# Kernel tuning notes

Hardware: AMD Instinct MI355X
Metric: run time of the kernel (lower is better)

Reference implementation:

```python
import jax, jax.numpy as jnp
import numpy as np

B, S, D, H, F = 2, 2048, 768, 12, 3072
HD = D // H


def setup_inputs() -> dict:
    key = jax.random.key(0)
    ks = jax.random.split(key, 6)
    g = lambda k, sh, sc: jax.random.normal(k, sh, jnp.float32) * sc
    return {
        "x": g(ks[0], (B, S, D), 1.0),
        "mask": jnp.tril(jnp.ones((1, 1, S, S), dtype=jnp.bool_)),  # causal
        "qkv_w": g(ks[1], (3 * D, D), 0.02),
        "qkv_b": jnp.zeros((3 * D,), jnp.float32),
        "out_w": g(ks[2], (D, D), 0.02),
        "out_b": jnp.zeros((D,), jnp.float32),
        "fc1_w": g(ks[3], (F, D), 0.02),
        "fc1_b": jnp.zeros((F,), jnp.float32),
        "fc2_w": g(ks[4], (D, F), 0.02),
        "fc2_b": jnp.zeros((D,), jnp.float32),
        "ln1_w": jnp.ones((D,), jnp.float32),
        "ln1_b": jnp.zeros((D,), jnp.float32),
        "ln2_w": jnp.ones((D,), jnp.float32),
        "ln2_b": jnp.zeros((D,), jnp.float32),
    }


def _layernorm(x, w, b, eps=1e-5):
    m = x.mean(-1, keepdims=True)
    v = ((x - m) ** 2).mean(-1, keepdims=True)
    return (x - m) * jax.lax.rsqrt(v + eps) * w + b


def reference(x, mask, qkv_w, qkv_b, out_w, out_b, fc1_w, fc1_b, fc2_w, fc2_b,
              ln1_w, ln1_b, ln2_w, ln2_b):
    b, s, d = x.shape
    h = d // HD  # num_heads
    # --- pre-norm multi-head self-attention (dropout = eval/identity) ---
    hx = _layernorm(x, ln1_w, ln1_b)
    qkv = hx @ qkv_w.T + qkv_b                      # [b,s,3d]
    qkv = qkv.reshape(b, s, 3, h, HD).transpose(2, 0, 3, 1, 4)  # [3,b,h,s,hd]
    q, k, v = qkv[0], qkv[1], qkv[2]
    scale = jnp.sqrt(jnp.float32(HD))
    scores = jnp.einsum("bhqd,bhkd->bhqk", q, k) / scale  # [b,h,s,s]
    scores = jnp.where(mask, scores, -jnp.inf)
    attn = jax.nn.softmax(scores, axis=-1)
    o = jnp.einsum("bhqk,bhkd->bhqd", attn, v)      # [b,h,s,hd]
    o = o.transpose(0, 2, 1, 3).reshape(b, s, d)
    x = x + (o @ out_w.T + out_b)
    # --- pre-norm GELU feed-forward ---
    h2 = _layernorm(x, ln2_w, ln2_b)
    ff = jax.nn.gelu(h2 @ fc1_w.T + fc1_b, approximate=False) @ fc2_w.T + fc2_b
    return x + ff
```

## Files before the change

kernel.cpp:

```cpp
#include <hip/hip_runtime.h>
#include <hip/hip_bf16.h>
#include <cstdint>
#include <cstddef>

typedef __bf16 bf16;
typedef unsigned short ushort_t;
typedef __attribute__((ext_vector_type(8))) __bf16 bf16x8;
typedef __attribute__((ext_vector_type(4))) __bf16 bf16x4;
typedef __attribute__((ext_vector_type(4))) float f32x4;

#define NB 2
#define NS 2048
#define ND 768
#define NH 12
#define NF 3072
#define NT (NB * NS)

__device__ __forceinline__ f32x4 mfma16(bf16x8 a, bf16x8 b, f32x4 c) {
  return __builtin_amdgcn_mfma_f32_16x16x32_bf16(a, b, c, 0, 0, 0);
}

__device__ __forceinline__ void gl_lds16(const bf16* g, bf16* l) {
  __builtin_amdgcn_global_load_lds(
      (__attribute__((address_space(1))) void*)(uintptr_t)g,
      (__attribute__((address_space(3))) void*)l,
      16, 0, 0);
}

__device__ __forceinline__ int xcd_swz(int lin, int nwg) {
  const int q = nwg >> 3, r = nwg & 7;
  const int x = lin & 7, i = lin >> 3;
  return (x < r ? x * (q + 1) : r * (q + 1) + (x - r) * q) + i;
}

__device__ __forceinline__ float gelu_fast(float v) {
  const float u = v * (0.7978845608028654f + 0.03567740814f * v * v);
  const float e = exp2f(u * 2.885390081777927f);
  return v - v / (1.f + e);
}

__global__ __launch_bounds__(256) void sniff_kernel(
    const ushort_t* __restrict__ x, int* __restrict__ flag) {
  __shared__ int s[4];
  int bad = 0;
  for (int i = threadIdx.x; i < 4096; i += 256) {
    const int e = (x[i] >> 7) & 0xFF;
    bad |= (e >= 0xC0);
  }
  bad = __any(bad) ? 1 : 0;
  if ((threadIdx.x & 63) == 0) s[threadIdx.x >> 6] = bad;
  __syncthreads();
  if (threadIdx.x == 0) *flag = s[0] | s[1] | s[2] | s[3];
}

struct CvtArgs {
  const void* s[8];
  bf16* d[8];
  int n8[8];
  int total8;
};

__global__ __launch_bounds__(256) void cvt_all(CvtArgs a,
                                               const int* __restrict__ flag) {
  const int isf = *flag;
  const int stride = gridDim.x * 256;
  for (int i = blockIdx.x * 256 + threadIdx.x; i < a.total8; i += stride) {
    int seg = 0, off = i;
    while (off >= a.n8[seg]) { off -= a.n8[seg]; ++seg; }
    bf16x8 o;
    if (isf) {
      const float* s = (const float*)a.s[seg] + (size_t)off * 8;
      const f32x4 f0 = *(const f32x4*)s;
      const f32x4 f1 = *(const f32x4*)(s + 4);
#pragma unroll
      for (int j = 0; j < 4; ++j) {
        o[j] = (bf16)f0[j];
        o[4 + j] = (bf16)f1[j];
      }
    } else {
      o = *((const bf16x8*)a.s[seg] + off);
    }
    *((bf16x8*)a.d[seg] + off) = o;
  }
}

__global__ __launch_bounds__(256) void ln_kernel(
    const void* __restrict__ xv, const void* __restrict__ wv,
    const void* __restrict__ bv, bf16* __restrict__ y,
    const int* __restrict__ flag) {
  const int isf = *flag;
  const int row = blockIdx.x * 4 + (threadIdx.x >> 6);
  const int L = threadIdx.x & 63;
  const float* xf = (const float*)xv;
  const bf16* xh = (const bf16*)xv;
  const float* wf = (const float*)wv;
  const bf16* wh = (const bf16*)wv;
  const float* bf_ = (const float*)bv;
  const bf16* bh = (const bf16*)bv;
  const size_t base = (size_t)row * ND;
  float v[12];
  float s = 0.f, s2 = 0.f;
#pragma unroll
  for (int i = 0; i < 12; ++i) {
    const int c = L + i * 64;
    v[i] = isf ? xf[base + c] : (float)xh[base + c];
    s += v[i];
    s2 += v[i] * v[i];
  }
#pragma unroll
  for (int off = 1; off < 64; off <<= 1) {
    s += __shfl_xor(s, off);
    s2 += __shfl_xor(s2, off);
  }
  const float mean = s * (1.f / 768.f);
  const float var = s2 * (1.f / 768.f) - mean * mean;
  const float rstd = rsqrtf(var + 1e-5f);
  bf16* yr = y + base;
#pragma unroll
  for (int i = 0; i < 12; ++i) {
    const int c = L + i * 64;
    const float ww = isf ? wf[c] : (float)wh[c];
    const float bb = isf ? bf_[c] : (float)bh[c];
    yr[c] = (bf16)((v[i] - mean) * rstd * ww + bb);
  }
}

__global__ __launch_bounds__(256) void vt_kernel(
    const bf16* __restrict__ qkv, bf16* __restrict__ vT) {
  const int bh = blockIdx.y;
  const int b = bh / NH, h = bh % NH;
  const int st = blockIdx.x;
  __shared__ bf16 Vs[64 * 72];
  const int tid = threadIdx.x;
  {
    const int r = tid >> 2, c = (tid & 3) * 16;
    const bf16* src =
        qkv + (size_t)(b * NS + st * 64 + r) * (3 * ND) + 2 * ND + h * 64 + c;
    *(bf16x8*)&Vs[r * 72 + c] = *(const bf16x8*)src;
    *(bf16x8*)&Vs[r * 72 + c + 8] = *(const bf16x8*)(src + 8);
  }
  __syncthreads();
  {
    const int hd = tid >> 2, t0 = (tid & 3) * 16;
    bf16x8 o0, o1;
#pragma unroll
    for (int j = 0; j < 8; ++j) {
      o0[j] = Vs[(t0 + j) * 72 + hd];
      o1[j] = Vs[(t0 + 8 + j) * 72 + hd];
    }
    bf16* dst = vT + ((size_t)bh * 64 + hd) * NS + st * 64 + t0;
    *(bf16x8*)dst = o0;
    *(bf16x8*)(dst + 8) = o1;
  }
}

template <int EPI>
__global__ __launch_bounds__(256) void gemm64(
    const bf16* __restrict__ A, const bf16* __restrict__ Bt,
    const bf16* __restrict__ bias, const void* resid, void* C,
    int N, int K, int row0, const int* __restrict__ flag) {
  constexpr int NBUF = 3;
  __shared__ bf16 As[NBUF][64 * 64];
  __shared__ bf16 Bs[NBUF][128 * 64];
  int isf = 0;
  if (EPI == 2) {
    isf = *flag;
    asm volatile("" ::"s"(isf));
  }
  const int tid = threadIdx.x;
  const int w = tid >> 6, L = tid & 63;
  const int lg = L >> 4, lc = L & 15;
  const int wm = (w >> 1) * 32, wn = (w & 1) * 64;
  const int nwg = gridDim.x * gridDim.y;
  const int lin = xcd_swz(blockIdx.y * gridDim.x + blockIdx.x, nwg);
  const int bm = lin / gridDim.x, bn = lin % gridDim.x;

  const bf16* Ab = A + (size_t)bm * 64 * K;
  const bf16* Bb = Bt + (size_t)bn * 128 * K;

  const int srw = tid >> 3;
  const int scw = ((tid & 7) ^ (srw & 7)) * 8;

  f32x4 acc[2][4];
#pragma unroll
  for (int i = 0; i < 2; ++i)
#pragma unroll
    for (int j = 0; j < 4; ++j) acc[i][j] = (f32x4){0.f, 0.f, 0.f, 0.f};

#define G64_STAGE(buf, kk)                                                  \
  do {                                                                      \
    gl_lds16(Ab + (size_t)srw * K + (kk) + scw, As[buf] + tid * 8);         \
    gl_lds16(Ab + (size_t)(srw + 32) * K + (kk) + scw,                      \
             As[buf] + 2048 + tid * 8);                                     \
    gl_lds16(Bb + (size_t)srw * K + (kk) + scw, Bs[buf] + tid * 8);         \
    gl_lds16(Bb + (size_t)(srw + 32) * K + (kk) + scw,                      \
             Bs[buf] + 2048 + tid * 8);                                     \
    gl_lds16(Bb + (size_t)(srw + 64) * K + (kk) + scw,                      \
             Bs[buf] + 4096 + tid * 8);                                     \
    gl_lds16(Bb + (size_t)(srw + 96) * K + (kk) + scw,                      \
             Bs[buf] + 6144 + tid * 8);                                     \
  } while (0)

#define G64_COMP(cb)                                                        \
  do {                                                                      \
    bf16x8 af[2][2], bfr[2][4];                                             \
    _Pragma("unroll") for (int kk2 = 0; kk2 < 2; ++kk2) {                   \
      _Pragma("unroll") for (int mt = 0; mt < 2; ++mt) {                    \
        const int ra = wm + mt * 16 + lc;                                   \
        af[kk2][mt] = *(const bf16x8*)&As[cb][ra * 64 +                     \
                                             (((kk2 * 4 + lg) ^ (ra & 7))   \
                                              << 3)];                       \
      }                                                                     \
      _Pragma("unroll") for (int nt = 0; nt < 4; ++nt) {                    \
        const int rb = wn + nt * 16 + lc;                                   \
        bfr[kk2][nt] = *(const bf16x8*)&Bs[cb][rb * 64 +                    \
                                              (((kk2 * 4 + lg) ^ (rb & 7))  \
                                               << 3)];                      \
      }                                                                     \
    }                                                                       \
    _Pragma("unroll") for (int kk2 = 0; kk2 < 2; ++kk2)                     \
        _Pragma("unroll") for (int mt = 0; mt < 2; ++mt)                    \
            _Pragma("unroll") for (int nt = 0; nt < 4; ++nt)                \
                acc[mt][nt] = mfma16(af[kk2][mt], bfr[kk2][nt],             \
                                     acc[mt][nt]);                          \
  } while (0)

  const int nk = K >> 6;
  G64_STAGE(0, 0);
  int cur = 0, stg = 1;
  int k = 0;
  for (; k < nk - 1; ++k) {
    G64_STAGE(stg, (k + 1) * 64);
    asm volatile("s_waitcnt vmcnt(6)" ::: "memory");
    asm volatile("s_barrier" ::: "memory");
    G64_COMP(cur);
    cur = (cur + 1 == NBUF) ? 0 : cur + 1;
    stg = (stg + 1 == NBUF) ? 0 : stg + 1;
  }
  __syncthreads();
  G64_COMP(cur);
#undef G64_STAGE
#undef G64_COMP

  const float* rf = (const float*)resid;
  const bf16* rh = (const bf16*)resid;
  float* Cf = (float*)C;
  bf16* Ch = (bf16*)C;
#pragma unroll
  for (int mt = 0; mt < 2; ++mt) {
#pragma unroll
    for (int nt = 0; nt < 4; ++nt) {
      const int col = bn * 128 + wn + nt * 16 + lc;
      const float bv = (float)bias[col];
#pragma unroll
      for (int r = 0; r < 4; ++r) {
        const int row = bm * 64 + wm + mt * 16 + lg * 4 + r;
        float v = acc[mt][nt][r] + bv;
        if (EPI == 1) v = gelu_fast(v);
        const size_t idx = (size_t)(row0 + row) * N + col;
        if (EPI == 2) {
          v += isf ? rf[idx] : (float)rh[idx];
          if (isf) Cf[idx] = v; else Ch[idx] = (bf16)v;
        } else {
          Ch[idx] = (bf16)v;
        }
      }
    }
  }
}

template <int EPI, int TM>
__global__ __launch_bounds__(256) void gemm_fast(
    const bf16* __restrict__ A, const bf16* __restrict__ Bt,
    const bf16* __restrict__ bias, const void* resid, void* C,
    int N, int K, int row0, const int* __restrict__ flag) {
  constexpr int NBUF = (TM == 64) ? 5 : 3;
  constexpr int LOOK = NBUF - 2;
  constexpr int MT = TM / 32;
  __shared__ bf16 As[NBUF][TM * 32];
  __shared__ bf16 Bs[NBUF][128 * 32];
  int isf = 0;
  if (EPI == 2) {
    isf = *flag;
    asm volatile("" ::"s"(isf));
  }
  const int tid = threadIdx.x;
  const int w = tid >> 6, L = tid & 63;
  const int lg = L >> 4, lc = L & 15;
  const int lgx = (lg ^ ((lc >> 1) & 3)) * 8;
  const int wm = (w >> 1) * (TM / 2), wn = (w & 1) * 64;
  const int nwg = gridDim.x * gridDim.y;
  const int lin = xcd_swz(blockIdx.y * gridDim.x + blockIdx.x, nwg);
  const int bm = lin / gridDim.x, bn = lin % gridDim.x;

  const bf16* Ab = A + (size_t)bm * TM * K;
  const bf16* Bb = Bt + (size_t)bn * 128 * K;

  const int sr = tid >> 2;
  const int sc = ((tid & 3) ^ ((tid >> 3) & 3)) * 8;

  f32x4 acc[MT][4];
#pragma unroll
  for (int i = 0; i < MT; ++i)
#pragma unroll
    for (int j = 0; j < 4; ++j) acc[i][j] = (f32x4){0.f, 0.f, 0.f, 0.f};

#define GF_STAGE(buf, kk)                                                   \
  do {                                                                      \
    gl_lds16(Ab + (size_t)sr * K + (kk) + sc, As[buf] + tid * 8);           \
    if (TM == 128)                                                          \
      gl_lds16(Ab + (size_t)(sr + 64) * K + (kk) + sc,                      \
               As[buf] + 2048 + tid * 8);                                   \
    gl_lds16(Bb + (size_t)sr * K + (kk) + sc, Bs[buf] + tid * 8);           \
    gl_lds16(Bb + (size_t)(sr + 64) * K + (kk) + sc,                        \
             Bs[buf] + 2048 + tid * 8);                                     \
  } while (0)

#define GF_COMP(cb)                                                         \
  do {                                                                      \
    bf16x8 af[MT], bfr[4];                                                  \
    _Pragma("unroll") for (int mt = 0; mt < MT; ++mt) af[mt] =              \
        *(const bf16x8*)&As[cb][(wm + mt * 16 + lc) * 32 + lgx];            \
    _Pragma("unroll") for (int nt = 0; nt < 4; ++nt) bfr[nt] =              \
        *(const bf16x8*)&Bs[cb][(wn + nt * 16 + lc) * 32 + lgx];            \
    _Pragma("unroll") for (int mt = 0; mt < MT; ++mt)                       \
        _Pragma("unroll") for (int nt = 0; nt < 4; ++nt) acc[mt][nt] =      \
            mfma16(af[mt], bfr[nt], acc[mt][nt]);                           \
  } while (0)

  const int nk = K >> 5;
#pragma unroll
  for (int s = 0; s < LOOK; ++s)
    if (s < nk) GF_STAGE(s, s * 32);
  int cur = 0, stg = LOOK;
  int k = 0;
  const int kmain = (nk > LOOK) ? nk - LOOK : 0;
  for (; k < kmain; ++k) {
    GF_STAGE(stg, (k + LOOK) * 32);
    if (TM == 64)
      asm volatile("s_waitcnt vmcnt(9)" ::: "memory");
    else
      asm volatile("s_waitcnt vmcnt(4)" ::: "memory");
    asm volatile("s_barrier" ::: "memory");
    GF_COMP(cur);
    cur = (cur + 1 == NBUF) ? 0 : cur + 1;
    stg = (stg + 1 == NBUF) ? 0 : stg + 1;
  }
  __syncthreads();
  for (; k < nk; ++k) {
    GF_COMP(cur);
    cur = (cur + 1 == NBUF) ? 0 : cur + 1;
  }
#undef GF_STAGE
#undef GF_COMP

  const float* rf = (const float*)resid;
  const bf16* rh = (const bf16*)resid;
  float* Cf = (float*)C;
  bf16* Ch = (bf16*)C;
#pragma unroll
  for (int mt = 0; mt < MT; ++mt) {
#pragma unroll
    for (int nt = 0; nt < 4; ++nt) {
      const int col = bn * 128 + wn + nt * 16 + lc;
      const float bv = (float)bias[col];
#pragma unroll
      for (int r = 0; r < 4; ++r) {
        const int row = bm * TM + wm + mt * 16 + lg * 4 + r;
        float v = acc[mt][nt][r] + bv;
        if (EPI == 1) v = gelu_fast(v);
        const size_t idx = (size_t)(row0 + row) * N + col;
        if (EPI == 2) {
          v += isf ? rf[idx] : (float)rh[idx];
          if (isf) Cf[idx] = v; else Ch[idx] = (bf16)v;
        } else {
          Ch[idx] = (bf16)v;
        }
      }
    }
  }
}

__global__ __launch_bounds__(256) void gemm_qkv(
    const bf16* __restrict__ A, const bf16* __restrict__ Bt,
    const bf16* __restrict__ bias, bf16* __restrict__ qkvout,
    bf16* __restrict__ vT) {
  const int K = ND, N = 3 * ND;
  constexpr int NBUF = 3;
  constexpr int LOOK = 1;
  __shared__ bf16 As[NBUF][128 * 32];
  __shared__ bf16 Bs[NBUF][128 * 32];
  const int tid = threadIdx.x;
  const int w = tid >> 6, L = tid & 63;
  const int lg = L >> 4, lc = L & 15;
  const int lgx = (lg ^ ((lc >> 1) & 3)) * 8;
  const int wm = (w >> 1) * 64, wn = (w & 1) * 64;
  const int nwg = gridDim.x * gridDim.y;
  const int lin = xcd_swz(blockIdx.y * gridDim.x + blockIdx.x, nwg);
  const int bm = lin / gridDim.x, bn = lin % gridDim.x;

  const bf16* Ab = A + (size_t)bm * 128 * K;
  const bf16* Bb = Bt + (size_t)bn * 128 * K;

  const int sr = tid >> 2;
  const int sc = ((tid & 3) ^ ((tid >> 3) & 3)) * 8;

  f32x4 acc[4][4];
#pragma unroll
  for (int i = 0; i < 4; ++i)
#pragma unroll
    for (int j = 0; j < 4; ++j) acc[i][j] = (f32x4){0.f, 0.f, 0.f, 0.f};

#define QKV_STAGE(buf, kk)                                                  \
  do {                                                                      \
    gl_lds16(Ab + (size_t)sr * K + (kk) + sc, As[buf] + tid * 8);           \
    gl_lds16(Ab + (size_t)(sr + 64) * K + (kk) + sc,                        \
             As[buf] + 2048 + tid * 8);                                     \
    gl_lds16(Bb + (size_t)sr * K + (kk) + sc, Bs[buf] + tid * 8);           \
    gl_lds16(Bb + (size_t)(sr + 64) * K + (kk) + sc,                        \
             Bs[buf] + 2048 + tid * 8);                                     \
  } while (0)

#define QKV_COMP(cb)                                                        \
  do {                                                                      \
    bf16x8 af[4], bfr[4];                                                   \
    _Pragma("unroll") for (int mt = 0; mt < 4; ++mt) af[mt] =               \
        *(const bf16x8*)&As[cb][(wm + mt * 16 + lc) * 32 + lgx];            \
    _Pragma("unroll") for (int nt = 0; nt < 4; ++nt) bfr[nt] =              \
        *(const bf16x8*)&Bs[cb][(wn + nt * 16 + lc) * 32 + lgx];            \
    _Pragma("unroll") for (int mt = 0; mt < 4; ++mt)                        \
        _Pragma("unroll") for (int nt = 0; nt < 4; ++nt) acc[mt][nt] =      \
            mfma16(af[mt], bfr[nt], acc[mt][nt]);                           \
  } while (0)

  const int nk = K >> 5;
  QKV_STAGE(0, 0);
  int cur = 0, stg = LOOK;
  int k = 0;
  const int kmain = nk - LOOK;
  for (; k < kmain; ++k) {
    QKV_STAGE(stg, (k + LOOK) * 32);
    asm volatile("s_waitcnt vmcnt(4)" ::: "memory");
    asm volatile("s_barrier" ::: "memory");
    QKV_COMP(cur);
    cur = (cur + 1 == NBUF) ? 0 : cur + 1;
    stg = (stg + 1 == NBUF) ? 0 : stg + 1;
  }
  __syncthreads();
  for (; k < nk; ++k) {
    QKV_COMP(cur);
    cur = (cur + 1 == NBUF) ? 0 : cur + 1;
  }
#undef QKV_STAGE
#undef QKV_COMP

#pragma unroll
  for (int mt = 0; mt < 4; ++mt) {
#pragma unroll
    for (int nt = 0; nt < 4; ++nt) {
      const int col = bn * 128 + wn + nt * 16 + lc;
      const float bv = (float)bias[col];
      if (col < 2 * ND) {
#pragma unroll
        for (int r = 0; r < 4; ++r) {
          const int row = bm * 128 + wm + mt * 16 + lg * 4 + r;
          qkvout[(size_t)row * N + col] = (bf16)(acc[mt][nt][r] + bv);
        }
      } else {
        const int colv = col - 2 * ND;
        const int h_ = colv >> 6, hd = colv & 63;
        bf16x4 pk;
#pragma unroll
        for (int r = 0; r < 4; ++r) pk[r] = (bf16)(acc[mt][nt][r] + bv);
        const int tok0 = bm * 128 + wm + mt * 16 + lg * 4;
        const int b_ = tok0 >> 11, s0 = tok0 & (NS - 1);
        *(bf16x4*)&vT[((size_t)(b_ * NH + h_) * 64 + hd) * NS + s0] = pk;
      }
    }
  }
}

template <int EPI>
__global__ __launch_bounds__(256) void gemm_bt(
    const bf16* __restrict__ A, const void* __restrict__ Bt,
    const void* __restrict__ bias, const void* resid, void* C,
    int N, int K, int row0, const int* __restrict__ flag) {
  __shared__ bf16 As[128 * 32];
  __shared__ bf16 Bs[128 * 32];
  const int isf = *flag;
  const int tid = threadIdx.x;
  const int w = tid >> 6, L = tid & 63;
  const int lg = L >> 4, lc = L & 15;
  const int wm = (w >> 1) * 64, wn = (w & 1) * 64;
  const int nwg = gridDim.x * gridDim.y;
  const int lin = xcd_swz(blockIdx.y * gridDim.x + blockIdx.x, nwg);
  const int bm = lin / gridDim.x, bn = lin % gridDim.x;

  const bf16* Ab = A + (size_t)bm * 128 * K;
  const bf16* Bth = (const bf16*)Bt + (size_t)bn * 128 * K;
  const float* Btf = (const float*)Bt + (size_t)bn * 128 * K;

  const int sr = tid >> 1;
  const int sc = (tid & 1) * 16;

  f32x4 acc[4][4];
#pragma unroll
  for (int i = 0; i < 4; ++i)
#pragma unroll
    for (int j = 0; j < 4; ++j) acc[i][j] = (f32x4){0.f, 0.f, 0.f, 0.f};

  for (int k0 = 0; k0 < K; k0 += 32) {
    const bf16* ap = Ab + (size_t)sr * K + k0 + sc;
    const bf16x8 a0 = *(const bf16x8*)ap;
    const bf16x8 a1 = *(const bf16x8*)(ap + 8);
    bf16x8 b0, b1;
    if (isf) {
      const float* bp = Btf + (size_t)sr * K + k0 + sc;
      const f32x4 f0 = *(const f32x4*)bp;
      const f32x4 f1 = *(const f32x4*)(bp + 4);
      const f32x4 f2 = *(const f32x4*)(bp + 8);
      const f32x4 f3 = *(const f32x4*)(bp + 12);
#pragma unroll
      for (int j = 0; j < 4; ++j) {
        b0[j] = (bf16)f0[j];
        b0[4 + j] = (bf16)f1[j];
        b1[j] = (bf16)f2[j];
        b1[4 + j] = (bf16)f3[j];
      }
    } else {
      const bf16* bp = Bth + (size_t)sr * K + k0 + sc;
      b0 = *(const bf16x8*)bp;
      b1 = *(const bf16x8*)(bp + 8);
    }
    __syncthreads();
    *(bf16x8*)&As[sr * 32 + sc] = a0;
    *(bf16x8*)&As[sr * 32 + sc + 8] = a1;
    *(bf16x8*)&Bs[sr * 32 + sc] = b0;
    *(bf16x8*)&Bs[sr * 32 + sc + 8] = b1;
    __syncthreads();

    bf16x8 af[4], bfr[4];
#pragma unroll
    for (int mt = 0; mt < 4; ++mt)
      af[mt] = *(const bf16x8*)&As[(wm + mt * 16 + lc) * 32 + lg * 8];
#pragma unroll
    for (int nt = 0; nt < 4; ++nt)
      bfr[nt] = *(const bf16x8*)&Bs[(wn + nt * 16 + lc) * 32 + lg * 8];
#pragma unroll
    for (int mt = 0; mt < 4; ++mt)
#pragma unroll
      for (int nt = 0; nt < 4; ++nt)
        acc[mt][nt] = mfma16(af[mt], bfr[nt], acc[mt][nt]);
  }

  const float* biasf = (const float*)bias;
  const bf16* biash = (const bf16*)bias;
  const float* rf = (const float*)resid;
  const bf16* rh = (const bf16*)resid;
  float* Cf = (float*)C;
  bf16* Ch = (bf16*)C;
#pragma unroll
  for (int mt = 0; mt < 4; ++mt) {
#pragma unroll
    for (int nt = 0; nt < 4; ++nt) {
      const int col = bn * 128 + wn + nt * 16 + lc;
      const float bv = isf ? biasf[col] : (float)biash[col];
#pragma unroll
      for (int r = 0; r < 4; ++r) {
        const int row = bm * 128 + wm + mt * 16 + lg * 4 + r;
        float v = acc[mt][nt][r] + bv;
        if (EPI == 1) v = gelu_fast(v);
        const size_t idx = (size_t)(row0 + row) * N + col;
        if (EPI == 2) {
          v += isf ? rf[idx] : (float)rh[idx];
          if (isf) Cf[idx] = v; else Ch[idx] = (bf16)v;
        } else {
          Ch[idx] = (bf16)v;
        }
      }
    }
  }
}

__global__ __launch_bounds__(128) void flash_attn_sp(
    const bf16* __restrict__ qkv, const bf16* __restrict__ vT,
    bf16* __restrict__ o, float* __restrict__ po, float* __restrict__ pl) {
  const int nwg = gridDim.x * gridDim.y;
  const int lin = xcd_swz(blockIdx.y * gridDim.x + blockIdx.x, nwg);
  const int bh = lin / 47;
  const int c = lin % 47;
  const int b = bh / NH, h = bh % NH;
  int qt, kt_lo, kt_hi, direct, cc = 0;
  if (c == 0) {
    qt = 16; kt_lo = 0; kt_hi = 16; direct = 1;
  } else if (c <= 30) {
    qt = 31 - ((c - 1) >> 1);
    const int hh = (qt + 1) >> 1;
    cc = (c - 1) & 1;
    if (cc) { kt_lo = hh; kt_hi = qt; }
    else    { kt_lo = 0;  kt_hi = hh - 1; }
    direct = 0;
  } else {
    qt = 46 - c; kt_lo = 0; kt_hi = qt; direct = 1;
  }
  const int q0 = qt * 64;
  const int tid = threadIdx.x;
  const int w = tid >> 6, L = tid & 63;
  const int lg = L >> 4, lc = L & 15;

  __shared__ bf16 Ks[64 * 72];
  __shared__ bf16 Vts[64 * 72];
  __shared__ bf16 Ps[2][32 * 72];

  const float QSCALE = 0.18033688011112042f;
  bf16x8 qf[2][2];
#pragma unroll
  for (int m = 0; m < 2; ++m) {
    const size_t tokq = (size_t)(b * NS + q0 + w * 32 + m * 16 + lc);
    const bf16* qp = qkv + tokq * (3 * ND) + h * 64 + lg * 8;
    const bf16x8 q0r = *(const bf16x8*)qp;
    const bf16x8 q1r = *(const bf16x8*)(qp + 32);
#pragma unroll
    for (int jj = 0; jj < 8; ++jj) {
      qf[m][0][jj] = (bf16)((float)q0r[jj] * QSCALE);
      qf[m][1][jj] = (bf16)((float)q1r[jj] * QSCALE);
    }
  }

  const int kr = tid >> 1, kc = (tid & 1) * 32;
  const bf16* kbase =
      qkv + (size_t)(b * NS + kr) * (3 * ND) + ND + h * 64 + kc;
  const bf16* vbase = vT + ((size_t)bh * 64 + kr) * NS + kc;

  f32x4 oacc[2][4];
#pragma unroll
  for (int m = 0; m < 2; ++m)
#pragma unroll
    for (int nt = 0; nt < 4; ++nt) oacc[m][nt] = (f32x4){0.f, 0.f, 0.f, 0.f};
  float lacc[2] = {0.f, 0.f};

  bf16x8 kreg[4], vreg[4];
  {
    const bf16* kn = kbase + (size_t)kt_lo * 64 * (3 * ND);
    const bf16* vn = vbase + (size_t)kt_lo * 64;
#pragma unroll
    for (int p = 0; p < 4; ++p) {
      kreg[p] = *(const bf16x8*)(kn + p * 8);
      vreg[p] = *(const bf16x8*)(vn + p * 8);
    }
  }

  for (int kt = kt_lo; kt <= kt_hi; ++kt) {
    __syncthreads();
#pragma unroll
    for (int p = 0; p < 4; ++p) {
      *(bf16x8*)&Ks[kr * 72 + kc + p * 8] = kreg[p];
      *(bf16x8*)&Vts[kr * 72 + kc + p * 8] = vreg[p];
    }
    __syncthreads();

    if (kt < kt_hi) {
      const bf16* kn = kbase + (size_t)(kt + 1) * 64 * (3 * ND);
      const bf16* vn = vbase + (size_t)(kt + 1) * 64;
#pragma unroll
      for (int p = 0; p < 4; ++p) {
        kreg[p] = *(const bf16x8*)(kn + p * 8);
        vreg[p] = *(const bf16x8*)(vn + p * 8);
      }
    }

    f32x4 s[2][4];
    __builtin_amdgcn_s_setprio(1);
#pragma unroll
    for (int nt = 0; nt < 4; ++nt) {
      const bf16x8 kb0 = *(const bf16x8*)&Ks[(nt * 16 + lc) * 72 + lg * 8];
      const bf16x8 kb1 =
          *(const bf16x8*)&Ks[(nt * 16 + lc) * 72 + 32 + lg * 8];
#pragma unroll
      for (int m = 0; m < 2; ++m) {
        f32x4 z = (f32x4){0.f, 0.f, 0.f, 0.f};
        s[m][nt] = mfma16(kb0, qf[m][0], z);
        s[m][nt] = mfma16(kb1, qf[m][1], s[m][nt]);
      }
    }
    __builtin_amdgcn_s_setprio(0);
    if (kt == qt) {
#pragma unroll
      for (int m = 0; m < 2; ++m)
#pragma unroll
        for (int nt = 0; nt < 4; ++nt)
#pragma unroll
          for (int r = 0; r < 4; ++r) {
            const int kv = nt * 16 + lg * 4 + r;
            const int qrow = w * 32 + m * 16 + lc;
            if (kv > qrow) s[m][nt][r] = -1.0e30f;
          }
    }
#pragma unroll
    for (int m = 0; m < 2; ++m)
#pragma unroll
      for (int nt = 0; nt < 4; ++nt) {
        bf16x4 pk;
#pragma unroll
        for (int r = 0; r < 4; ++r) {
          const float p = exp2f(fminf(s[m][nt][r], 20.f));
          lacc[m] += p;
          pk[r] = (bf16)p;
        }
        *(bf16x4*)&Ps[w][(m * 16 + lc) * 72 + nt * 16 + lg * 4] = pk;
      }
    bf16x8 pa[2][2];
#pragma unroll
    for (int m = 0; m < 2; ++m) {
      pa[m][0] = *(const bf16x8*)&Ps[w][(m * 16 + lc) * 72 + lg * 8];
      pa[m][1] = *(const bf16x8*)&Ps[w][(m * 16 + lc) * 72 + 32 + lg * 8];
    }
    __builtin_amdgcn_s_setprio(1);
#pragma unroll
    for (int nt = 0; nt < 4; ++nt) {
      const bf16x8 v0 = *(const bf16x8*)&Vts[(nt * 16 + lc) * 72 + lg * 8];
      const bf16x8 v1 =
          *(const bf16x8*)&Vts[(nt * 16 + lc) * 72 + 32 + lg * 8];
#pragma unroll
      for (int m = 0; m < 2; ++m) {
        oacc[m][nt] = mfma16(pa[m][0], v0, oacc[m][nt]);
        oacc[m][nt] = mfma16(pa[m][1], v1, oacc[m][nt]);
      }
    }
    __builtin_amdgcn_s_setprio(0);
  }

#pragma unroll
  for (int m = 0; m < 2; ++m) {
    lacc[m] += __shfl_xor(lacc[m], 16);
    lacc[m] += __shfl_xor(lacc[m], 32);
  }

  if (direct) {
    float lr[2][4];
#pragma unroll
    for (int m = 0; m < 2; ++m)
#pragma unroll
      for (int r = 0; r < 4; ++r) lr[m][r] = __shfl(lacc[m], lg * 4 + r);
#pragma unroll
    for (int m = 0; m < 2; ++m)
#pragma unroll
      for (int nt = 0; nt < 4; ++nt)
#pragma unroll
        for (int r = 0; r < 4; ++r) {
          const int qrow = q0 + w * 32 + m * 16 + lg * 4 + r;
          const float val = oacc[m][nt][r] / lr[m][r];
          o[(size_t)(b * NS + qrow) * ND + h * 64 + nt * 16 + lc] =
              (bf16)val;
        }
  } else {
    const int slot = qt - 17;
    float* pob = po + (((size_t)(bh * 15 + slot)) * 2 + cc) * 4096;
#pragma unroll
    for (int m = 0; m < 2; ++m)
#pragma unroll
      for (int nt = 0; nt < 4; ++nt)
#pragma unroll
        for (int r = 0; r < 4; ++r) {
          const int row = w * 32 + m * 16 + lg * 4 + r;
          const int col = nt * 16 + lc;
          pob[row * 64 + col] = oacc[m][nt][r];
        }
    if (L < 16) {
      float* plb = pl + ((bh * 15 + slot) * 2 + cc) * 64;
      plb[w * 32 + L] = lacc[0];
      plb[w * 32 + 16 + L] = lacc[1];
    }
  }
}

__global__ __launch_bounds__(256) void attn_combine(
    const float* __restrict__ po, const float* __restrict__ pl,
    bf16* __restrict__ o) {
  const int slot = blockIdx.x;
  const int bh = blockIdx.y;
  const int qt = slot + 17;
  const int b = bh / NH, h = bh % NH;
  const float* poA = po + ((size_t)(bh * 15 + slot)) * 2 * 4096;
  const float* poB = poA + 4096;
  const float* plA = pl + (bh * 15 + slot) * 2 * 64;
  const float* plB = plA + 64;
  for (int e = threadIdx.x; e < 4096; e += 256) {
    const int q = e >> 6, hd = e & 63;
    const float val = (poA[e] + poB[e]) / (plA[q] + plB[q]);
    o[(size_t)(b * NS + qt * 64 + q) * ND + h * 64 + hd] = (bf16)val;
  }
}

__global__ __launch_bounds__(128) void flash_attn_v7(
    const bf16* __restrict__ qkv, const bf16* __restrict__ vT,
    bf16* __restrict__ o) {
  const int nwg = gridDim.x * gridDim.y;
  const int lin = xcd_swz(blockIdx.y * gridDim.x + blockIdx.x, nwg);
  const int xcd = lin / 96;
  const int i96 = lin % 96;
  const int bl = i96 >> 5;
  const int j = i96 & 31;
  const int bh = xcd * 3 + bl;
  const int b = bh / NH, h = bh % NH;
  int qt;
  if (bl == 0) qt = j;
  else if (bl == 1) qt = (j + 16) & 31;
  else qt = (j < 16) ? (31 - 2 * j) : (62 - 2 * j);
  const int q0 = qt * 64;
  const int tid = threadIdx.x;
  const int w = tid >> 6, L = tid & 63;
  const int lg = L >> 4, lc = L & 15;

  __shared__ bf16 Ks[2][64 * 72];
  __shared__ bf16 Vts[2][64 * 72];
  __shared__ bf16 Ps[2][32 * 72];

  const float QSCALE = 0.18033688011112042f;
  bf16x8 qf[2][2];
#pragma unroll
  for (int m = 0; m < 2; ++m) {
    const size_t tokq = (size_t)(b * NS + q0 + w * 32 + m * 16 + lc);
    const bf16* qp = qkv + tokq * (3 * ND) + h * 64 + lg * 8;
    const bf16x8 q0r = *(const bf16x8*)qp;
    const bf16x8 q1r = *(const bf16x8*)(qp + 32);
#pragma unroll
    for (int jj = 0; jj < 8; ++jj) {
      qf[m][0][jj] = (bf16)((float)q0r[jj] * QSCALE);
      qf[m][1][jj] = (bf16)((float)q1r[jj] * QSCALE);
    }
  }

  const int kr = tid >> 1, kc = (tid & 1) * 32;
  const bf16* kbase =
      qkv + (size_t)(b * NS + kr) * (3 * ND) + ND + h * 64 + kc;
  const bf16* vbase = vT + ((size_t)bh * 64 + kr) * NS + kc;

  f32x4 oacc[2][4];
#pragma unroll
  for (int m = 0; m < 2; ++m)
#pragma unroll
    for (int nt = 0; nt < 4; ++nt) oacc[m][nt] = (f32x4){0.f, 0.f, 0.f, 0.f};
  float lacc[2] = {0.f, 0.f};

  const int nkt = qt + 1;

  bf16x8 kreg[4], vreg[4];
#pragma unroll
  for (int p = 0; p < 4; ++p) {
    kreg[p] = *(const bf16x8*)(kbase + p * 8);
    vreg[p] = *(const bf16x8*)(vbase + p * 8);
  }
#pragma unroll
  for (int p = 0; p < 4; ++p) {
    *(bf16x8*)&Ks[0][kr * 72 + kc + p * 8] = kreg[p];
    *(bf16x8*)&Vts[0][kr * 72 + kc + p * 8] = vreg[p];
  }

  for (int kt = 0; kt < nkt; ++kt) {
    __syncthreads();
    const int cur = kt & 1;

    if (kt + 1 < nkt) {
      const bf16* kn = kbase + (size_t)(kt + 1) * 64 * (3 * ND);
      const bf16* vn = vbase + (size_t)(kt + 1) * 64;
#pragma unroll
      for (int p = 0; p < 4; ++p) {
        kreg[p] = *(const bf16x8*)(kn + p * 8);
        vreg[p] = *(const bf16x8*)(vn + p * 8);
      }
    }

    f32x4 s[2][4];
    __builtin_amdgcn_s_setprio(1);
#pragma unroll
    for (int nt = 0; nt < 4; ++nt) {
      const bf16x8 kb0 =
          *(const bf16x8*)&Ks[cur][(nt * 16 + lc) * 72 + lg * 8];
      const bf16x8 kb1 =
          *(const bf16x8*)&Ks[cur][(nt * 16 + lc) * 72 + 32 + lg * 8];
#pragma unroll
      for (int m = 0; m < 2; ++m) {
        f32x4 z = (f32x4){0.f, 0.f, 0.f, 0.f};
        s[m][nt] = mfma16(kb0, qf[m][0], z);
        s[m][nt] = mfma16(kb1, qf[m][1], s[m][nt]);
      }
    }
    __builtin_amdgcn_s_setprio(0);
    if (kt == nkt - 1) {
#pragma unroll
      for (int m = 0; m < 2; ++m)
#pragma unroll
        for (int nt = 0; nt < 4; ++nt)
#pragma unroll
          for (int r = 0; r < 4; ++r) {
            const int kv = nt * 16 + lg * 4 + r;
            const int qrow = w * 32 + m * 16 + lc;
            if (kv > qrow) s[m][nt][r] = -1.0e30f;
          }
    }
#pragma unroll
    for (int m = 0; m < 2; ++m)
#pragma unroll
      for (int nt = 0; nt < 4; ++nt) {
        bf16x4 pk;
#pragma unroll
        for (int r = 0; r < 4; ++r) {
          const float p = exp2f(fminf(s[m][nt][r], 20.f));
          lacc[m] += p;
          pk[r] = (bf16)p;
        }
        *(bf16x4*)&Ps[w][(m * 16 + lc) * 72 + nt * 16 + lg * 4] = pk;
      }
    bf16x8 pa[2][2];
#pragma unroll
    for (int m = 0; m < 2; ++m) {
      pa[m][0] = *(const bf16x8*)&Ps[w][(m * 16 + lc) * 72 + lg * 8];
      pa[m][1] = *(const bf16x8*)&Ps[w][(m * 16 + lc) * 72 + 32 + lg * 8];
    }

    if (kt + 1 < nkt) {
      const int nxt = cur ^ 1;
#pragma unroll
      for (int p = 0; p < 4; ++p) {
        *(bf16x8*)&Ks[nxt][kr * 72 + kc + p * 8] = kreg[p];
        *(bf16x8*)&Vts[nxt][kr * 72 + kc + p * 8] = vreg[p];
      }
    }

    __builtin_amdgcn_s_setprio(1);
#pragma unroll
    for (int nt = 0; nt < 4; ++nt) {
      const bf16x8 v0 =
          *(const bf16x8*)&Vts[cur][(nt * 16 + lc) * 72 + lg * 8];
      const bf16x8 v1 =
          *(const bf16x8*)&Vts[cur][(nt * 16 + lc) * 72 + 32 + lg * 8];
#pragma unroll
      for (int m = 0; m < 2; ++m) {
        oacc[m][nt] = mfma16(pa[m][0], v0, oacc[m][nt]);
        oacc[m][nt] = mfma16(pa[m][1], v1, oacc[m][nt]);
      }
    }
    __builtin_amdgcn_s_setprio(0);
  }

#pragma unroll
  for (int m = 0; m < 2; ++m) {
    lacc[m] += __shfl_xor(lacc[m], 16);
    lacc[m] += __shfl_xor(lacc[m], 32);
  }
  float lr[2][4];
#pragma unroll
  for (int m = 0; m < 2; ++m)
#pragma unroll
    for (int r = 0; r < 4; ++r) lr[m][r] = __shfl(lacc[m], lg * 4 + r);

#pragma unroll
  for (int m = 0; m < 2; ++m)
#pragma unroll
    for (int nt = 0; nt < 4; ++nt)
#pragma unroll
      for (int r = 0; r < 4; ++r) {
        const int qrow = q0 + w * 32 + m * 16 + lg * 4 + r;
        const float val = oacc[m][nt][r] / lr[m][r];
        o[(size_t)(b * NS + qrow) * ND + h * 64 + nt * 16 + lc] = (bf16)val;
      }
}

__global__ __launch_bounds__(256) void flash_attn_v1(
    const bf16* __restrict__ qkv, bf16* __restrict__ o) {
  const int bh = blockIdx.y;
  const int b = bh / NH, h = bh % NH;
  const int qt = gridDim.x - 1 - blockIdx.x;
  const int q0 = qt * 64;
  const int tid = threadIdx.x;
  const int w = tid >> 6, L = tid & 63;
  const int lg = L >> 4, lc = L & 15;

  __shared__ bf16 Ks[64 * 72];
  __shared__ bf16 Vts[64 * 72];
  __shared__ bf16 Ps[4][16 * 72];

  const float QSCALE = 0.18033688011112042f;
  const size_t tokq = (size_t)(b * NS + q0 + w * 16 + lc);
  const bf16* qp = qkv + tokq * (3 * ND) + h * 64 + lg * 8;
  const bf16x8 qr0 = *(const bf16x8*)qp;
  const bf16x8 qr1 = *(const bf16x8*)(qp + 32);
  bf16x8 qf0, qf1;
#pragma unroll
  for (int j = 0; j < 8; ++j) {
    qf0[j] = (bf16)((float)qr0[j] * QSCALE);
    qf1[j] = (bf16)((float)qr1[j] * QSCALE);
  }

  f32x4 oacc[4];
#pragma unroll
  for (int nt = 0; nt < 4; ++nt) oacc[nt] = (f32x4){0.f, 0.f, 0.f, 0.f};
  float lacc[4] = {0.f, 0.f, 0.f, 0.f};

  for (int kt = 0; kt <= qt; ++kt) {
    __syncthreads();
#pragma unroll
    for (int p = 0; p < 2; ++p) {
      const int r = (p * 256 + tid) >> 3;
      const int c = (tid & 7) * 8;
      const bf16* kp =
          qkv + (size_t)(b * NS + kt * 64 + r) * (3 * ND) + ND + h * 64 + c;
      const bf16x8 k8 = *(const bf16x8*)kp;
      *(bf16x8*)&Ks[r * 72 + c] = k8;
      const bf16x8 v8 = *(const bf16x8*)(kp + ND);
#pragma unroll
      for (int j = 0; j < 8; ++j) Vts[(c + j) * 72 + r] = v8[j];
    }
    __syncthreads();

    f32x4 s[4];
#pragma unroll
    for (int nt = 0; nt < 4; ++nt) {
      const bf16x8 b0 = *(const bf16x8*)&Ks[(nt * 16 + lc) * 72 + lg * 8];
      const bf16x8 b1 = *(const bf16x8*)&Ks[(nt * 16 + lc) * 72 + 32 + lg * 8];
      f32x4 z = (f32x4){0.f, 0.f, 0.f, 0.f};
      s[nt] = mfma16(qf0, b0, z);
      s[nt] = mfma16(qf1, b1, s[nt]);
    }
    if (kt == qt) {
#pragma unroll
      for (int nt = 0; nt < 4; ++nt)
#pragma unroll
        for (int r = 0; r < 4; ++r) {
          const int qrow = w * 16 + lg * 4 + r;
          const int kcol = nt * 16 + lc;
          if (kcol > qrow) s[nt][r] = -1.0e30f;
        }
    }
#pragma unroll
    for (int nt = 0; nt < 4; ++nt)
#pragma unroll
      for (int r = 0; r < 4; ++r) {
        const float p = exp2f(fminf(s[nt][r], 20.f));
        lacc[r] += p;
        Ps[w][(lg * 4 + r) * 72 + nt * 16 + lc] = (bf16)p;
      }
    __syncthreads();

    const bf16x8 p0 = *(const bf16x8*)&Ps[w][lc * 72 + lg * 8];
    const bf16x8 p1 = *(const bf16x8*)&Ps[w][lc * 72 + 32 + lg * 8];
#pragma unroll
    for (int nt = 0; nt < 4; ++nt) {
      const bf16x8 v0 = *(const bf16x8*)&Vts[(nt * 16 + lc) * 72 + lg * 8];
      const bf16x8 v1 = *(const bf16x8*)&Vts[(nt * 16 + lc) * 72 + 32 + lg * 8];
      oacc[nt] = mfma16(p0, v0, oacc[nt]);
      oacc[nt] = mfma16(p1, v1, oacc[nt]);
    }
  }

#pragma unroll
  for (int msk = 1; msk < 16; msk <<= 1)
#pragma unroll
    for (int r = 0; r < 4; ++r) lacc[r] += __shfl_xor(lacc[r], msk);

#pragma unroll
  for (int nt = 0; nt < 4; ++nt)
#pragma unroll
    for (int r = 0; r < 4; ++r) {
      const int qrow = q0 + w * 16 + lg * 4 + r;
      const float val = oacc[nt][r] / lacc[r];
      o[(size_t)(b * NS + qrow) * ND + h * 64 + nt * 16 + lc] = (bf16)val;
    }
}

extern "C" void kernel_launch(void* const* d_in, const int* in_sizes, int n_in,
                              void* d_out, int out_size, void* d_ws,
                              size_t ws_size, hipStream_t stream) {
  const void* x = d_in[0];
  const void* qkv_w = d_in[2];
  const void* qkv_b = d_in[3];
  const void* out_w = d_in[4];
  const void* out_b = d_in[5];
  const void* fc1_w = d_in[6];
  const void* fc1_b = d_in[7];
  const void* fc2_w = d_in[8];
  const void* fc2_b = d_in[9];
  const void* ln1_w = d_in[10];
  const void* ln1_b = d_in[11];
  const void* ln2_w = d_in[12];
  const void* ln2_b = d_in[13];
  (void)in_sizes; (void)n_in; (void)out_size;

  char* ws = (char*)d_ws;
  int* flag = (int*)ws;

  sniff_kernel<<<dim3(1), 256, 0, stream>>>((const ushort_t*)x, flag);

  const size_t T1 = 58210048, T2 = 51918592, T3 = 45627136, T4 = 39335680;

  if (ws_size >= T2) {
    bf16* wq = (bf16*)(ws + 256);
    bf16* wo = wq + 1769472;
    bf16* w1 = wo + 589824;
    bf16* w2 = w1 + 2359296;
    bf16* bq = w2 + 2359296;
    bf16* bo = bq + 2304;
    bf16* b1 = bo + 768;
    bf16* b2 = b1 + 3072;
    bf16* slotA = b2 + 768;
    bf16* vT = slotA + (size_t)NT * ND;
    bf16* slotB = vT + (size_t)NT * ND;
    bf16* hx = slotA, *oat = slotA, *h2 = slotA;
    bf16* qkv = slotB;
    float* po = (float*)(ws + 45627136);
    float* pl = po + (size_t)24 * 15 * 2 * 4096;
    const bool sp = ws_size >= T1;

    CvtArgs ca;
    ca.s[0] = qkv_w; ca.d[0] = wq; ca.n8[0] = 1769472 / 8;
    ca.s[1] = out_w; ca.d[1] = wo; ca.n8[1] = 589824 / 8;
    ca.s[2] = fc1_w; ca.d[2] = w1; ca.n8[2] = 2359296 / 8;
    ca.s[3] = fc2_w; ca.d[3] = w2; ca.n8[3] = 2359296 / 8;
    ca.s[4] = qkv_b; ca.d[4] = bq; ca.n8[4] = 2304 / 8;
    ca.s[5] = out_b; ca.d[5] = bo; ca.n8[5] = 768 / 8;
    ca.s[6] = fc1_b; ca.d[6] = b1; ca.n8[6] = 3072 / 8;
    ca.s[7] = fc2_b; ca.d[7] = b2; ca.n8[7] = 768 / 8;
    ca.total8 = (1769472 + 589824 + 2359296 + 2359296 + 2304 + 768 + 3072 +
                 768) / 8;
    cvt_all<<<dim3(880), 256, 0, stream>>>(ca, flag);

    ln_kernel<<<dim3(NT / 4), 256, 0, stream>>>(x, ln1_w, ln1_b, hx, flag);
    gemm_qkv<<<dim3(18, 32), 256, 0, stream>>>(hx, wq, bq, qkv, vT);
    if (sp) {
      flash_attn_sp<<<dim3(47, 24), 128, 0, stream>>>(qkv, vT, oat, po, pl);
      attn_combine<<<dim3(15, 24), 256, 0, stream>>>(po, pl, oat);
    } else {
      flash_attn_v7<<<dim3(NS / 64, NB * NH), 128, 0, stream>>>(qkv, vT, oat);
    }
    gemm64<2><<<dim3(6, 64), 256, 0, stream>>>(
        oat, wo, bo, x, d_out, ND, ND, 0, flag);
    ln_kernel<<<dim3(NT / 4), 256, 0, stream>>>(d_out, ln2_w, ln2_b, h2, flag);
    if (ws_size >= T1) {
      bf16* ff1 = slotB;
      gemm64<1><<<dim3(24, 64), 256, 0, stream>>>(
          h2, w1, b1, nullptr, ff1, NF, ND, 0, flag);
      gemm64<2><<<dim3(6, 64), 256, 0, stream>>>(
          ff1, w2, b2, d_out, d_out, ND, NF, 0, flag);
    } else {
      bf16* ff1c = slotB;
      for (int c = 0; c < 2; ++c) {
        gemm64<1><<<dim3(24, 32), 256, 0, stream>>>(
            h2 + (size_t)c * 2048 * ND, w1, b1, nullptr, ff1c, NF, ND, 0, flag);
        gemm64<2><<<dim3(6, 32), 256, 0, stream>>>(
            ff1c, w2, b2, d_out, d_out, ND, NF, c * 2048, flag);
      }
    }
  } else if (ws_size >= T4) {
    bf16* wq = (bf16*)(ws + 256);
    bf16* wo = wq + 1769472;
    bf16* w1 = wo + 589824;
    bf16* w2 = w1 + 2359296;
    bf16* bq = w2 + 2359296;
    bf16* bo = bq + 2304;
    bf16* b1 = bo + 768;
    bf16* b2 = b1 + 3072;
    bf16* slotA = b2 + 768;
    bf16* slotB = slotA + (size_t)NT * ND;
    bf16* hx = slotA, *oat = slotA, *h2 = slotA;
    bf16* qkv = slotB;

    CvtArgs ca;
    ca.s[0] = qkv_w; ca.d[0] = wq; ca.n8[0] = 1769472 / 8;
    ca.s[1] = out_w; ca.d[1] = wo; ca.n8[1] = 589824 / 8;
    ca.s[2] = fc1_w; ca.d[2] = w1; ca.n8[2] = 2359296 / 8;
    ca.s[3] = fc2_w; ca.d[3] = w2; ca.n8[3] = 2359296 / 8;
    ca.s[4] = qkv_b; ca.d[4] = bq; ca.n8[4] = 2304 / 8;
    ca.s[5] = out_b; ca.d[5] = bo; ca.n8[5] = 768 / 8;
    ca.s[6] = fc1_b; ca.d[6] = b1; ca.n8[6] = 3072 / 8;
    ca.s[7] = fc2_b; ca.d[7] = b2; ca.n8[7] = 768 / 8;
    ca.total8 = (1769472 + 589824 + 2359296 + 2359296 + 2304 + 768 + 3072 +
                 768) / 8;
    cvt_all<<<dim3(880), 256, 0, stream>>>(ca, flag);

    ln_kernel<<<dim3(NT / 4), 256, 0, stream>>>(x, ln1_w, ln1_b, hx, flag);
    gemm_fast<0, 128><<<dim3(18, 32), 256, 0, stream>>>(
        hx, wq, bq, nullptr, qkv, 3 * ND, ND, 0, flag);
    flash_attn_v1<<<dim3(NS / 64, NB * NH), 256, 0, stream>>>(qkv, oat);
    gemm64<2><<<dim3(6, 64), 256, 0, stream>>>(
        oat, wo, bo, x, d_out, ND, ND, 0, flag);
    ln_kernel<<<dim3(NT / 4), 256, 0, stream>>>(d_out, ln2_w, ln2_b, h2, flag);
    if (ws_size >= T3) {
      bf16* ff1 = slotB;
      gemm64<1><<<dim3(24, 64), 256, 0, stream>>>(
          h2, w1, b1, nullptr, ff1, NF, ND, 0, flag);
      gemm64<2><<<dim3(6, 64), 256, 0, stream>>>(
          ff1, w2, b2, d_out, d_out, ND, NF, 0, flag);
    } else {
      bf16* ff1c = slotB;
      for (int c = 0; c < 2; ++c) {
        gemm64<1><<<dim3(24, 32), 256, 0, stream>>>(
            h2 + (size_t)c * 2048 * ND, w1, b1, nullptr, ff1c, NF, ND, 0, flag);
        gemm64<2><<<dim3(6, 32), 256, 0, stream>>>(
            ff1c, w2, b2, d_out, d_out, ND, NF, c * 2048, flag);
      }
    }
  } else {
    const size_t szTD = (size_t)NT * ND * sizeof(bf16);
    bf16* slotA = (bf16*)(ws + 256);
    bf16* qkv = (bf16*)(ws + 256 + szTD);
    bf16* hx = slotA, *oat = slotA, *h2 = slotA;
    bf16* ff1c = qkv;

    ln_kernel<<<dim3(NT / 4), 256, 0, stream>>>(x, ln1_w, ln1_b, hx, flag);
    gemm_bt<0><<<dim3(18, 32), 256, 0, stream>>>(
        hx, qkv_w, qkv_b, nullptr, qkv, 3 * ND, ND, 0, flag);
    flash_attn_v1<<<dim3(NS / 64, NB * NH), 256, 0, stream>>>(qkv, oat);
    gemm_bt<2><<<dim3(6, 32), 256, 0, stream>>>(
        oat, out_w, out_b, x, d_out, ND, ND, 0, flag);
    ln_kernel<<<dim3(NT / 4), 256, 0, stream>>>(d_out, ln2_w, ln2_b, h2, flag);
    for (int c = 0; c < 4; ++c) {
      gemm_bt<1><<<dim3(24, 8), 256, 0, stream>>>(
          h2 + (size_t)c * 1024 * ND, fc1_w, fc1_b, nullptr, ff1c, NF, ND, 0,
          flag);
      gemm_bt<2><<<dim3(6, 8), 256, 0, stream>>>(
          ff1c, fc2_w, fc2_b, d_out, d_out, ND, NF, c * 1024, flag);
    }
  }
}
```

Measured before the change: 311.4 us.

## Replace QKV GEMM with 64-row tile, 64-wide K-step kernel

The QKV projection GEMM moves from 128x128 tiles with a 32-wide K step to 64x128 tiles with a 64-wide K step and a new 8-way XOR LDS swizzle. The grid doubles to 1152 workgroups, which gives better CU occupancy and load balance, and each workgroup now runs half as many pipeline iterations and barriers. In exchange, each tile reuses data less and reads more global memory, and LDS use per block rises.

```diff
diff --git a/kernel.cpp b/kernel.cpp
--- a/kernel.cpp
+++ b/kernel.cpp
@@ -269,6 +269,115 @@
   }
 }
 
+__global__ __launch_bounds__(256) void gemm_qkv64(
+    const bf16* __restrict__ A, const bf16* __restrict__ Bt,
+    const bf16* __restrict__ bias, bf16* __restrict__ qkvout,
+    bf16* __restrict__ vT) {
+  const int K = ND, N = 3 * ND;
+  constexpr int NBUF = 3;
+  __shared__ bf16 As[NBUF][64 * 64];
+  __shared__ bf16 Bs[NBUF][128 * 64];
+  const int tid = threadIdx.x;
+  const int w = tid >> 6, L = tid & 63;
+  const int lg = L >> 4, lc = L & 15;
+  const int wm = (w >> 1) * 32, wn = (w & 1) * 64;
+  const int nwg = gridDim.x * gridDim.y;
+  const int lin = xcd_swz(blockIdx.y * gridDim.x + blockIdx.x, nwg);
+  const int bm = lin / gridDim.x, bn = lin % gridDim.x;
+
+  const bf16* Ab = A + (size_t)bm * 64 * K;
+  const bf16* Bb = Bt + (size_t)bn * 128 * K;
+
+  const int srw = tid >> 3;
+  const int scw = ((tid & 7) ^ (srw & 7)) * 8;
+
+  f32x4 acc[2][4];
+#pragma unroll
+  for (int i = 0; i < 2; ++i)
+#pragma unroll
+    for (int j = 0; j < 4; ++j) acc[i][j] = (f32x4){0.f, 0.f, 0.f, 0.f};
+
+#define Q64_STAGE(buf, kk)                                                  \
+  do {                                                                      \
+    gl_lds16(Ab + (size_t)srw * K + (kk) + scw, As[buf] + tid * 8);         \
+    gl_lds16(Ab + (size_t)(srw + 32) * K + (kk) + scw,                      \
+             As[buf] + 2048 + tid * 8);                                     \
+    gl_lds16(Bb + (size_t)srw * K + (kk) + scw, Bs[buf] + tid * 8);         \
+    gl_lds16(Bb + (size_t)(srw + 32) * K + (kk) + scw,                      \
+             Bs[buf] + 2048 + tid * 8);                                     \
+    gl_lds16(Bb + (size_t)(srw + 64) * K + (kk) + scw,                      \
+             Bs[buf] + 4096 + tid * 8);                                     \
+    gl_lds16(Bb + (size_t)(srw + 96) * K + (kk) + scw,                      \
+             Bs[buf] + 6144 + tid * 8);                                     \
+  } while (0)
+
+#define Q64_COMP(cb)                                                        \
+  do {                                                                      \
+    bf16x8 af[2][2], bfr[2][4];                                             \
+    _Pragma("unroll") for (int kk2 = 0; kk2 < 2; ++kk2) {                   \
+      _Pragma("unroll") for (int mt = 0; mt < 2; ++mt) {                    \
+        const int ra = wm + mt * 16 + lc;                                   \
+        af[kk2][mt] = *(const bf16x8*)&As[cb][ra * 64 +                     \
+                                             (((kk2 * 4 + lg) ^ (ra & 7))   \
+                                              << 3)];                       \
+      }                                                                     \
+      _Pragma("unroll") for (int nt = 0; nt < 4; ++nt) {                    \
+        const int rb = wn + nt * 16 + lc;                                   \
+        bfr[kk2][nt] = *(const bf16x8*)&Bs[cb][rb * 64 +                    \
+                                              (((kk2 * 4 + lg) ^ (rb & 7))  \
+                                               << 3)];                      \
+      }                                                                     \
+    }                                                                       \
+    _Pragma("unroll") for (int kk2 = 0; kk2 < 2; ++kk2)                     \
+        _Pragma("unroll") for (int mt = 0; mt < 2; ++mt)                    \
+            _Pragma("unroll") for (int nt = 0; nt < 4; ++nt)                \
+                acc[mt][nt] = mfma16(af[kk2][mt], bfr[kk2][nt],             \
+                                     acc[mt][nt]);                          \
+  } while (0)
+
+  const int nk = K >> 6;
+  Q64_STAGE(0, 0);
+  int cur = 0, stg = 1;
+  int k = 0;
+  for (; k < nk - 1; ++k) {
+    Q64_STAGE(stg, (k + 1) * 64);
+    asm volatile("s_waitcnt vmcnt(6)" ::: "memory");
+    asm volatile("s_barrier" ::: "memory");
+    Q64_COMP(cur);
+    cur = (cur + 1 == NBUF) ? 0 : cur + 1;
+    stg = (stg + 1 == NBUF) ? 0 : stg + 1;
+  }
+  __syncthreads();
+  Q64_COMP(cur);
+#undef Q64_STAGE
+#undef Q64_COMP
+
+#pragma unroll
+  for (int mt = 0; mt < 2; ++mt) {
+#pragma unroll
+    for (int nt = 0; nt < 4; ++nt) {
+      const int col = bn * 128 + wn + nt * 16 + lc;
+      const float bv = (float)bias[col];
+      if (col < 2 * ND) {
+#pragma unroll
+        for (int r = 0; r < 4; ++r) {
+          const int row = bm * 64 + wm + mt * 16 + lg * 4 + r;
+          qkvout[(size_t)row * N + col] = (bf16)(acc[mt][nt][r] + bv);
+        }
+      } else {
+        const int colv = col - 2 * ND;
+        const int h_ = colv >> 6, hd = colv & 63;
+        bf16x4 pk;
+#pragma unroll
+        for (int r = 0; r < 4; ++r) pk[r] = (bf16)(acc[mt][nt][r] + bv);
+        const int tok0 = bm * 64 + wm + mt * 16 + lg * 4;
+        const int b_ = tok0 >> 11, s0 = tok0 & (NS - 1);
+        *(bf16x4*)&vT[((size_t)(b_ * NH + h_) * 64 + hd) * NS + s0] = pk;
+      }
+    }
+  }
+}
+
 template <int EPI, int TM>
 __global__ __launch_bounds__(256) void gemm_fast(
     const bf16* __restrict__ A, const bf16* __restrict__ Bt,
@@ -376,105 +485,6 @@
         } else {
           Ch[idx] = (bf16)v;
         }
-      }
-    }
-  }
-}
-
-__global__ __launch_bounds__(256) void gemm_qkv(
-    const bf16* __restrict__ A, const bf16* __restrict__ Bt,
-    const bf16* __restrict__ bias, bf16* __restrict__ qkvout,
-    bf16* __restrict__ vT) {
-  const int K = ND, N = 3 * ND;
-  constexpr int NBUF = 3;
-  constexpr int LOOK = 1;
-  __shared__ bf16 As[NBUF][128 * 32];
-  __shared__ bf16 Bs[NBUF][128 * 32];
-  const int tid = threadIdx.x;
-  const int w = tid >> 6, L = tid & 63;
-  const int lg = L >> 4, lc = L & 15;
-  const int lgx = (lg ^ ((lc >> 1) & 3)) * 8;
-  const int wm = (w >> 1) * 64, wn = (w & 1) * 64;
-  const int nwg = gridDim.x * gridDim.y;
-  const int lin = xcd_swz(blockIdx.y * gridDim.x + blockIdx.x, nwg);
-  const int bm = lin / gridDim.x, bn = lin % gridDim.x;
-
-  const bf16* Ab = A + (size_t)bm * 128 * K;
-  const bf16* Bb = Bt + (size_t)bn * 128 * K;
-
-  const int sr = tid >> 2;
-  const int sc = ((tid & 3) ^ ((tid >> 3) & 3)) * 8;
-
-  f32x4 acc[4][4];
-#pragma unroll
-  for (int i = 0; i < 4; ++i)
-#pragma unroll
-    for (int j = 0; j < 4; ++j) acc[i][j] = (f32x4){0.f, 0.f, 0.f, 0.f};
-
-#define QKV_STAGE(buf, kk)                                                  \
-  do {                                                                      \
-    gl_lds16(Ab + (size_t)sr * K + (kk) + sc, As[buf] + tid * 8);           \
-    gl_lds16(Ab + (size_t)(sr + 64) * K + (kk) + sc,                        \
-             As[buf] + 2048 + tid * 8);                                     \
-    gl_lds16(Bb + (size_t)sr * K + (kk) + sc, Bs[buf] + tid * 8);           \
-    gl_lds16(Bb + (size_t)(sr + 64) * K + (kk) + sc,                        \
-             Bs[buf] + 2048 + tid * 8);                                     \
-  } while (0)
-
-#define QKV_COMP(cb)                                                        \
-  do {                                                                      \
-    bf16x8 af[4], bfr[4];                                                   \
-    _Pragma("unroll") for (int mt = 0; mt < 4; ++mt) af[mt] =               \
-        *(const bf16x8*)&As[cb][(wm + mt * 16 + lc) * 32 + lgx];            \
-    _Pragma("unroll") for (int nt = 0; nt < 4; ++nt) bfr[nt] =              \
-        *(const bf16x8*)&Bs[cb][(wn + nt * 16 + lc) * 32 + lgx];            \
-    _Pragma("unroll") for (int mt = 0; mt < 4; ++mt)                        \
-        _Pragma("unroll") for (int nt = 0; nt < 4; ++nt) acc[mt][nt] =      \
-            mfma16(af[mt], bfr[nt], acc[mt][nt]);                           \
-  } while (0)
-
-  const int nk = K >> 5;
-  QKV_STAGE(0, 0);
-  int cur = 0, stg = LOOK;
-  int k = 0;
-  const int kmain = nk - LOOK;
-  for (; k < kmain; ++k) {
-    QKV_STAGE(stg, (k + LOOK) * 32);
-    asm volatile("s_waitcnt vmcnt(4)" ::: "memory");
-    asm volatile("s_barrier" ::: "memory");
-    QKV_COMP(cur);
-    cur = (cur + 1 == NBUF) ? 0 : cur + 1;
-    stg = (stg + 1 == NBUF) ? 0 : stg + 1;
-  }
-  __syncthreads();
-  for (; k < nk; ++k) {
-    QKV_COMP(cur);
-    cur = (cur + 1 == NBUF) ? 0 : cur + 1;
-  }
-#undef QKV_STAGE
-#undef QKV_COMP
-
-#pragma unroll
-  for (int mt = 0; mt < 4; ++mt) {
-#pragma unroll
-    for (int nt = 0; nt < 4; ++nt) {
-      const int col = bn * 128 + wn + nt * 16 + lc;
-      const float bv = (float)bias[col];
-      if (col < 2 * ND) {
-#pragma unroll
-        for (int r = 0; r < 4; ++r) {
-          const int row = bm * 128 + wm + mt * 16 + lg * 4 + r;
-          qkvout[(size_t)row * N + col] = (bf16)(acc[mt][nt][r] + bv);
-        }
-      } else {
-        const int colv = col - 2 * ND;
-        const int h_ = colv >> 6, hd = colv & 63;
-        bf16x4 pk;
-#pragma unroll
-        for (int r = 0; r < 4; ++r) pk[r] = (bf16)(acc[mt][nt][r] + bv);
-        const int tok0 = bm * 128 + wm + mt * 16 + lg * 4;
-        const int b_ = tok0 >> 11, s0 = tok0 & (NS - 1);
-        *(bf16x4*)&vT[((size_t)(b_ * NH + h_) * 64 + hd) * NS + s0] = pk;
       }
     }
   }
@@ -1126,7 +1136,7 @@
     cvt_all<<<dim3(880), 256, 0, stream>>>(ca, flag);
 
     ln_kernel<<<dim3(NT / 4), 256, 0, stream>>>(x, ln1_w, ln1_b, hx, flag);
-    gemm_qkv<<<dim3(18, 32), 256, 0, stream>>>(hx, wq, bq, qkv, vT);
+    gemm_qkv64<<<dim3(18, 64), 256, 0, stream>>>(hx, wq, bq, qkv, vT);
     if (sp) {
       flash_attn_sp<<<dim3(47, 24), 128, 0, stream>>>(qkv, vT, oat, po, pl);
       attn_combine<<<dim3(15, 24), 256, 0, stream>>>(po, pl, oat);
```

Result: no change. 312.3 us (+0.3%).
